# Optimization experiments

Measured on AMD Instinct MI355X. Metric: run time of the kernel, lower is better.

The kernel has to match this reference:

```python
import jax, jax.numpy as jnp
import numpy as np

B, P, D, H, L = 1024, 22, 3, 64, 4
HS = P + 1  # 22-dim one-hot atom type + 1 time channel
N = B * P


def _edges():
    # fully-connected directed edges (no self loops) per graph, batched with node offsets
    idx = np.arange(P)
    r, c = np.meshgrid(idx, idx, indexing='ij')
    m = r != c
    r0, c0 = r[m], c[m]
    off = (P * np.arange(B))[:, None]
    row = (r0[None, :] + off).reshape(-1)
    col = (c0[None, :] + off).reshape(-1)
    return row.astype(np.int32), col.astype(np.int32)


def setup_inputs() -> dict:
    key = jax.random.key(0)
    ks = jax.random.split(key, 12)
    s = 0.02
    row, col = _edges()
    return dict(
        input_array=jax.random.normal(ks[0], (B, P * D), jnp.float32),
        time_array=jax.random.uniform(ks[1], (B,), jnp.float32),
        emb_w=jax.random.normal(ks[2], (HS, H), jnp.float32) * s,
        emb_b=jnp.zeros((H,), jnp.float32),
        edge_w1=jax.random.normal(ks[3], (L, 2 * H + 2, H), jnp.float32) * s,
        edge_b1=jnp.zeros((L, H), jnp.float32),
        edge_w2=jax.random.normal(ks[4], (L, H, H), jnp.float32) * s,
        edge_b2=jnp.zeros((L, H), jnp.float32),
        node_w1=jax.random.normal(ks[5], (L, 2 * H, H), jnp.float32) * s,
        node_b1=jnp.zeros((L, H), jnp.float32),
        node_w2=jax.random.normal(ks[6], (L, H, H), jnp.float32) * s,
        node_b2=jnp.zeros((L, H), jnp.float32),
        cm_w1=jax.random.normal(ks[7], (L, H, H), jnp.float32) * s,
        cm_b1=jnp.zeros((L, H), jnp.float32),
        cm_w2=jax.random.normal(ks[8], (L, H, 1), jnp.float32) * 0.001,  # xavier gain=0.001 final layer
        cc_w1=jax.random.normal(ks[9], (L, H, H), jnp.float32) * s,
        cc_b1=jnp.zeros((L, H), jnp.float32),
        cc_w2=jax.random.normal(ks[10], (L, H, 1), jnp.float32) * 0.001,
        row=jnp.asarray(row),
        col=jnp.asarray(col),
    )


def reference(input_array, time_array, emb_w, emb_b, edge_w1, edge_b1, edge_w2, edge_b2,
              node_w1, node_b1, node_w2, node_b2, cm_w1, cm_b1, cm_w2,
              cc_w1, cc_b1, cc_w2, row, col):
    silu = jax.nn.silu
    x0 = input_array.reshape(N, D)
    # h_initial: one-hot atom types repeated over batch, plus time channel
    h = jnp.tile(jnp.eye(P, dtype=input_array.dtype), (B, 1))  # [N, 22]
    t = jnp.repeat(time_array[:, None], P, axis=1).reshape(N, 1)
    h = jnp.concatenate([h, t], axis=1)  # [N, 23]
    # edge_attr = squared distance at initial coords (fixed across layers)
    edge_attr = jnp.sum((x0[row] - x0[col]) ** 2, axis=1, keepdims=True)  # [E,1]
    h = h @ emb_w + emb_b  # embedding
    x = x0
    seg = lambda d: jax.ops.segment_sum(d, row, num_segments=N)
    for l in range(L):
        diff = x[row] - x[col]                                   # [E,3]
        radial = jnp.sum(diff ** 2, axis=1, keepdims=True)       # [E,1]
        coord_diff = diff / (jnp.sqrt(radial + 1e-8) + 1)
        e_in = jnp.concatenate([h[row], h[col], radial, edge_attr], axis=1)
        ef = silu(silu(e_in @ edge_w1[l] + edge_b1[l]) @ edge_w2[l] + edge_b2[l])  # [E,H]
        cross = jnp.cross(x[row], x[col])                        # [E,3]
        cross = cross / (jnp.sqrt(jnp.sum(cross ** 2, axis=1, keepdims=True) + 1e-8) + 1)
        cm = silu(ef @ cm_w1[l] + cm_b1[l]) @ cm_w2[l]           # [E,1]
        cc = silu(ef @ cc_w1[l] + cc_b1[l]) @ cc_w2[l]           # [E,1]
        trans = coord_diff * cm + cc * cross                     # [E,3]
        x = x + seg(trans)                                       # agg='sum'
        agg = jnp.concatenate([h, seg(ef)], axis=1)              # [N,2H]
        h = h + (silu(agg @ node_w1[l] + node_b1[l]) @ node_w2[l] + node_b2[l])  # recurrent
    vel = (x - x0).reshape(B, P, D)
    vel = vel - jnp.mean(vel, axis=1, keepdims=True)  # remove_mean
    return vel.reshape(B, P * D)
```

## Files before the change

### kernel.cpp

```cpp
#include <hip/hip_runtime.h>
#include <hip/hip_bf16.h>
#include <math.h>

#define PP 22
#define HH 64
#define NL 4
#define NE 462
#define NTILE 29
#define SST 68

typedef __attribute__((ext_vector_type(8))) short bf16x8;
typedef __attribute__((ext_vector_type(4))) float f32x4;

#define MFMA(A, B, C) __builtin_amdgcn_mfma_f32_16x16x32_bf16(A, B, C, 0, 0, 0)
#define PHI(mt, r) ((((mt) >> 1) << 5) + (((r) >> 2) << 3) + (((mt) & 1) << 2) + ((r) & 3))
#define WAVE_SYNC() asm volatile("s_waitcnt lgkmcnt(0)" ::: "memory")

__device__ __forceinline__ float silu_f(float v) { return v / (1.0f + __expf(-v)); }

__device__ __forceinline__ unsigned short f2bf(float x) {
    __hip_bfloat16 h = __float2bfloat16(x);
    unsigned short u;
    __builtin_memcpy(&u, &h, 2);
    return u;
}

#define LD8(dst, PTR) { \
    float4 _a = *(const float4*)(PTR); float4 _b = *(const float4*)((PTR) + 4); \
    dst[0]=_a.x; dst[1]=_a.y; dst[2]=_a.z; dst[3]=_a.w; \
    dst[4]=_b.x; dst[5]=_b.y; dst[6]=_b.z; dst[7]=_b.w; }

__global__ __launch_bounds__(64) void prep_w(
    const float* __restrict__ edge_w1, const float* __restrict__ edge_w2,
    const float* __restrict__ cm_w1, const float* __restrict__ cc_w1,
    const float* __restrict__ node_w1, const float* __restrict__ node_w2,
    unsigned short* __restrict__ ws)
{
    int blk = blockIdx.x;
    int l = blk >> 6, moff = blk & 63;
    int lane = threadIdx.x, n0 = lane & 15, kg = lane >> 4;
    const float* base; int col, kt;
    if (moff < 8)       { kt = moff >> 2;              int nt = moff & 3;        base = edge_w1 + l * 130 * HH;           col = nt * 16 + n0; }
    else if (moff < 16) { int m = moff - 8;  kt = m >> 2; int nt = m & 3;        base = edge_w1 + l * 130 * HH + 64 * HH; col = nt * 16 + n0; }
    else if (moff < 24) { int m = moff - 16; kt = m >> 2; int mt = m & 3;        base = edge_w2 + l * HH * HH;            col = PHI(mt, n0); }
    else if (moff < 32) { int m = moff - 24; kt = m >> 2; int nt = m & 3;        base = cm_w1 + l * HH * HH;              col = nt * 16 + n0; }
    else if (moff < 40) { int m = moff - 32; kt = m >> 2; int nt = m & 3;        base = cc_w1 + l * HH * HH;              col = nt * 16 + n0; }
    else if (moff < 56) { int m = moff - 40; kt = m >> 2; int mt = m & 3;        base = node_w1 + l * 128 * HH;           col = PHI(mt, n0); }
    else                { int m = moff - 56; kt = m >> 2; int nt = m & 3;        base = node_w2 + l * HH * HH;            col = nt * 16 + n0; }
    int k0 = kt * 32 + kg * 8;
    unsigned short* d = ws + blk * 512 + lane * 8;
#pragma unroll
    for (int j = 0; j < 8; ++j) d[j] = f2bf(base[(k0 + j) * HH + col]);
}

__global__ __launch_bounds__(512, 2) void egnn_kernel(
    const float* __restrict__ input, const float* __restrict__ timev,
    const float* __restrict__ emb_w, const float* __restrict__ emb_b,
    const float* __restrict__ edge_w1, const float* __restrict__ edge_b1,
    const float* __restrict__ edge_b2,
    const float* __restrict__ node_b1, const float* __restrict__ node_b2,
    const float* __restrict__ cm_b1, const float* __restrict__ cm_w2,
    const float* __restrict__ cc_b1, const float* __restrict__ cc_w2,
    const unsigned short* __restrict__ wfr,
    float* __restrict__ out)
{
    const int g0   = blockIdx.x * 2;
    const int tid  = threadIdx.x;
    const int w    = tid >> 6;
    const int lw   = w & 3;
    const int gi   = w >> 2;
    const int lane = tid & 63;
    const int n0   = lane & 15;
    const int kg   = lane >> 4;

    __shared__ __align__(16) unsigned short wlds[12288];
    __shared__ float sApre[2][PP][SST], sBpre[2][PP][SST];
    __shared__ float sh[2][PP][SST], sSeg[2][PP][SST];
    __shared__ __align__(16) float sx[2][PP][4];
    __shared__ __align__(16) float sx0[2][PP][4];
    __shared__ float sTr[2][PP][4];
    __shared__ float sW128[HH], sW129[HH];
    __shared__ float sBp[128];
    __shared__ float sHC[256];
    __shared__ float swPm[8][16], swPc[8][16];
    __shared__ float smean[2][3];

#define STAGE(SRC, N16) { const uint4* _s = (const uint4*)(SRC); uint4* _d = (uint4*)wlds; \
    for (int idx = tid; idx < (N16); idx += 512) _d[idx] = _s[idx]; }

    if (tid < 2 * PP * 3) {
        int gg = tid / (PP * 3), j = tid % (PP * 3);
        float v = input[(g0 + gg) * (PP * 3) + j];
        sx0[gg][j / 3][j % 3] = v;
        sx [gg][j / 3][j % 3] = v;
    }
    if (tid < 2 * PP) { int gg = tid / PP, p = tid % PP; sx0[gg][p][3] = 0.f; sx[gg][p][3] = 0.f; }
    {
        float tg = timev[g0 + gi];
        for (int i = lw; i < PP; i += 4)
            sh[gi][i][lane] = emb_w[i * HH + lane] + tg * emb_w[PP * HH + lane] + emb_b[lane];
    }
    for (int idx = tid; idx < 2 * PP * SST; idx += 512) (&sSeg[0][0][0])[idx] = 0.f;
    if (tid < 2 * PP * 4) (&sTr[0][0][0])[tid] = 0.f;
    __syncthreads();

    for (int l = 0; l < NL; ++l) {
        const unsigned short* wfl = wfr + (size_t)l * 32768;

        STAGE(wfl, 1024);
        if (tid < HH)               sW128[tid]        = edge_w1[(l * 130 + 128) * HH + tid];
        else if (tid < 2 * HH)      sW129[tid - HH]   = edge_w1[(l * 130 + 129) * HH + tid - HH];
        else if (tid < 2 * HH + 128) {
            int t2 = tid - 2 * HH;
            int i = t2 & 63, mt = i >> 4, r = i & 15;
            int phi = PHI(mt, r);
            sBp[t2] = (t2 < 64) ? edge_b2[l * HH + phi] : node_b1[l * HH + phi];
        } else if (tid < 2 * HH + 128 + 256) {
            int t3 = tid - (2 * HH + 128);
            int i = t3 & 63, arr = t3 >> 6;
            const float* src = (arr == 0) ? cm_b1 : (arr == 1) ? cc_b1 : (arr == 2) ? cm_w2 : cc_w2;
            sHC[t3] = src[l * HH + i];
        }
        __syncthreads();

        {
            int mtn = lw & 1, mat = lw >> 1;
            int node = mtn * 16 + n0;
            bool vn = node < PP;
            int crow = vn ? node : 0;
            bf16x8 hhi[2];
#pragma unroll
            for (int kt = 0; kt < 2; ++kt) {
                float vv[8];
                LD8(vv, &sh[gi][crow][kt * 32 + kg * 8]);
#pragma unroll
                for (int j = 0; j < 8; ++j)
                    hhi[kt][j] = (short)f2bf(vn ? vv[j] : 0.f);
            }
#pragma unroll
            for (int ntf = 0; ntf < 4; ++ntf) {
                f32x4 acc = (f32x4){0.f, 0.f, 0.f, 0.f};
#pragma unroll
                for (int kt = 0; kt < 2; ++kt) {
                    bf16x8 wv = *(const bf16x8*)&wlds[(mat * 8 + kt * 4 + ntf) * 512 + lane * 8];
                    acc = MFMA(hhi[kt], wv, acc);
                }
                int col = ntf * 16 + n0;
                float b1v = edge_b1[l * HH + col];
#pragma unroll
                for (int q = 0; q < 4; ++q) {
                    int m = mtn * 16 + kg * 4 + q;
                    if (m < PP) {
                        if (mat == 0) sApre[gi][m][col] = acc[q] + b1v;
                        else          sBpre[gi][m][col] = acc[q];
                    }
                }
            }
        }
        __syncthreads();

        STAGE(wfl + 16 * 512, 1536);
        __syncthreads();

        for (int jt = lw; jt < NTILE; jt += 4) {
            int e0 = jt * 16;
            int e = e0 + n0;
            bool vr = e < NE;
            int ec = vr ? e : (NE - 1);
            int a = ec % PP, r = ec / PP;
            int b = (r < a) ? r : r + 1;
            float4 xa = *(const float4*)&sx[gi][a][0];
            float4 xb = *(const float4*)&sx[gi][b][0];
            float4 oa = *(const float4*)&sx0[gi][a][0];
            float4 ob = *(const float4*)&sx0[gi][b][0];
            float dx = xa.x - xb.x, dy = xa.y - xb.y, dz = xa.z - xb.z;
            float rad = dx * dx + dy * dy + dz * dz;
            float ex = oa.x - ob.x, ey = oa.y - ob.y, ez = oa.z - ob.z;
            float ea = ex * ex + ey * ey + ez * ez;
            float inv = 1.0f / (sqrtf(rad + 1e-8f) + 1.0f);
            float cdx = dx * inv, cdy = dy * inv, cdz = dz * inv;
            float cx = xa.y * xb.z - xa.z * xb.y;
            float cy = xa.z * xb.x - xa.x * xb.z;
            float cz = xa.x * xb.y - xa.y * xb.x;
            float cn = 1.0f / (sqrtf(cx * cx + cy * cy + cz * cz + 1e-8f) + 1.0f);
            float crx = cx * cn, cry = cy * cn, crz = cz * cn;

            f32x4 acc[4];
#pragma unroll
            for (int mt = 0; mt < 4; ++mt) acc[mt] = (f32x4){0.f, 0.f, 0.f, 0.f};
#pragma unroll
            for (int kt = 0; kt < 2; ++kt) {
                int base = kt * 32 + kg * 8;
                float av[8], bv[8], w8[8], w9[8];
                LD8(av, &sApre[gi][a][base]);
                LD8(bv, &sBpre[gi][b][base]);
                LD8(w8, &sW128[base]);
                LD8(w9, &sW129[base]);
                bf16x8 zhi;
#pragma unroll
                for (int j8 = 0; j8 < 8; ++j8) {
                    float z = av[j8] + bv[j8] + rad * w8[j8] + ea * w9[j8];
                    zhi[j8] = (short)f2bf(silu_f(z));
                }
#pragma unroll
                for (int mt = 0; mt < 4; ++mt) {
                    bf16x8 wv = *(const bf16x8*)&wlds[(kt * 4 + mt) * 512 + lane * 8];
                    acc[mt] = MFMA(wv, zhi, acc[mt]);
                }
            }
            unsigned short pkE[4][4];
#pragma unroll
            for (int mt = 0; mt < 4; ++mt) {
                int phib = ((mt >> 1) << 5) + (kg << 3) + ((mt & 1) << 2);
#pragma unroll
                for (int q = 0; q < 4; ++q) {
                    float v = silu_f(acc[mt][q] + sBp[mt * 16 + kg * 4 + q]);
                    v = vr ? v : 0.f;
                    pkE[mt][q] = f2bf(v);
                    if (vr) atomicAdd(&sSeg[gi][a][phib + q], v);
                }
            }
            bf16x8 ehi[2];
#pragma unroll
            for (int kt = 0; kt < 2; ++kt)
#pragma unroll
                for (int j8 = 0; j8 < 8; ++j8)
                    ehi[kt][j8] = (short)pkE[kt * 2 + (j8 >> 2)][j8 & 3];

            float pm[4] = {0.f, 0.f, 0.f, 0.f}, pc[4] = {0.f, 0.f, 0.f, 0.f};
#pragma unroll
            for (int nt = 0; nt < 4; ++nt) {
                f32x4 am = (f32x4){0.f, 0.f, 0.f, 0.f};
                f32x4 ac = (f32x4){0.f, 0.f, 0.f, 0.f};
#pragma unroll
                for (int kt = 0; kt < 2; ++kt) {
                    bf16x8 cmw = *(const bf16x8*)&wlds[(8 + kt * 4 + nt) * 512 + lane * 8];
                    bf16x8 ccw = *(const bf16x8*)&wlds[(16 + kt * 4 + nt) * 512 + lane * 8];
                    am = MFMA(ehi[kt], cmw, am);
                    ac = MFMA(ehi[kt], ccw, ac);
                }
                float cmb = sHC[nt * 16 + n0];
                float ccb = sHC[64 + nt * 16 + n0];
                float cm2 = sHC[128 + nt * 16 + n0];
                float cc2 = sHC[192 + nt * 16 + n0];
#pragma unroll
                for (int q = 0; q < 4; ++q) {
                    pm[q] += silu_f(am[q] + cmb) * cm2;
                    pc[q] += silu_f(ac[q] + ccb) * cc2;
                }
            }
#pragma unroll
            for (int q = 0; q < 4; ++q) {
#pragma unroll
                for (int off = 1; off <= 8; off <<= 1) {
                    pm[q] += __shfl_xor(pm[q], off);
                    pc[q] += __shfl_xor(pc[q], off);
                }
            }
            if (n0 == 0) {
#pragma unroll
                for (int q = 0; q < 4; ++q) {
                    swPm[w][kg * 4 + q] = pm[q];
                    swPc[w][kg * 4 + q] = pc[q];
                }
            }
            WAVE_SYNC();
            float pmv = swPm[w][n0];
            float pcv = swPc[w][n0];
            if (kg == 0 && vr) {
                atomicAdd(&sTr[gi][a][0], cdx * pmv + pcv * crx);
                atomicAdd(&sTr[gi][a][1], cdy * pmv + pcv * cry);
                atomicAdd(&sTr[gi][a][2], cdz * pmv + pcv * crz);
            }
            WAVE_SYNC();
        }
        __syncthreads();

        STAGE(wfl + 40 * 512, 1536);
        __syncthreads();

        unsigned short pkN[4][4];
        {
            int mtn = lw >> 1;
            int node = mtn * 16 + n0;
            bool vn = node < PP;
            int crow = vn ? node : 0;
            f32x4 acc[4];
#pragma unroll
            for (int mt = 0; mt < 4; ++mt) acc[mt] = (f32x4){0.f, 0.f, 0.f, 0.f};
#pragma unroll
            for (int kt = 0; kt < 4; ++kt) {
                const float* srcp = (kt < 2) ? &sh[gi][crow][kt * 32 + kg * 8]
                                             : &sSeg[gi][crow][(kt - 2) * 32 + kg * 8];
                float vv[8];
                LD8(vv, srcp);
                bf16x8 bhi;
#pragma unroll
                for (int j8 = 0; j8 < 8; ++j8)
                    bhi[j8] = (short)f2bf(vn ? vv[j8] : 0.f);
#pragma unroll
                for (int mt = 0; mt < 4; ++mt) {
                    bf16x8 wv = *(const bf16x8*)&wlds[(kt * 4 + mt) * 512 + lane * 8];
                    acc[mt] = MFMA(wv, bhi, acc[mt]);
                }
            }
#pragma unroll
            for (int mt = 0; mt < 4; ++mt)
#pragma unroll
                for (int q = 0; q < 4; ++q)
                    pkN[mt][q] = f2bf(silu_f(acc[mt][q] + sBp[64 + mt * 16 + kg * 4 + q]));
        }
        __syncthreads();

        {
            bf16x8 mh[2];
#pragma unroll
            for (int kt = 0; kt < 2; ++kt)
#pragma unroll
                for (int j8 = 0; j8 < 8; ++j8)
                    mh[kt][j8] = (short)pkN[kt * 2 + (j8 >> 2)][j8 & 3];
            int mtn = lw >> 1;
#pragma unroll
            for (int t = 0; t < 2; ++t) {
                int ntf = (lw & 1) * 2 + t;
                f32x4 acc = (f32x4){0.f, 0.f, 0.f, 0.f};
#pragma unroll
                for (int kt = 0; kt < 2; ++kt) {
                    bf16x8 wv = *(const bf16x8*)&wlds[(16 + kt * 4 + ntf) * 512 + lane * 8];
                    acc = MFMA(mh[kt], wv, acc);
                }
                int col = ntf * 16 + n0;
                float nb2 = node_b2[l * HH + col];
#pragma unroll
                for (int q = 0; q < 4; ++q) {
                    int m = mtn * 16 + kg * 4 + q;
                    if (m < PP) sh[gi][m][col] += acc[q] + nb2;
                }
            }
        }
        if (tid < 2 * PP * 4) {
            int gg = tid / (PP * 4), j = tid % (PP * 4);
            int p = j >> 2, d = j & 3;
            float v = sTr[gg][p][d];
            if (d < 3) sx[gg][p][d] += v;
            sTr[gg][p][d] = 0.f;
        }
        for (int idx = tid; idx < 2 * PP * SST; idx += 512) (&sSeg[0][0][0])[idx] = 0.f;
        __syncthreads();
    }

    if (tid < 6) {
        int gg = tid / 3, d = tid % 3;
        float s = 0.0f;
        for (int p = 0; p < PP; ++p) s += sx[gg][p][d] - sx0[gg][p][d];
        smean[gg][d] = s / (float)PP;
    }
    __syncthreads();
    if (tid < 2 * PP * 3) {
        int gg = tid / (PP * 3), j = tid % (PP * 3);
        int p = j / 3, d = j % 3;
        out[(g0 + gg) * (PP * 3) + j] = (sx[gg][p][d] - sx0[gg][p][d]) - smean[gg][d];
    }
#undef STAGE
}

extern "C" void kernel_launch(void* const* d_in, const int* in_sizes, int n_in,
                              void* d_out, int out_size, void* d_ws, size_t ws_size,
                              hipStream_t stream) {
    const float* input   = (const float*)d_in[0];
    const float* timev   = (const float*)d_in[1];
    const float* emb_w   = (const float*)d_in[2];
    const float* emb_b   = (const float*)d_in[3];
    const float* edge_w1 = (const float*)d_in[4];
    const float* edge_b1 = (const float*)d_in[5];
    const float* edge_w2 = (const float*)d_in[6];
    const float* edge_b2 = (const float*)d_in[7];
    const float* node_w1 = (const float*)d_in[8];
    const float* node_b1 = (const float*)d_in[9];
    const float* node_w2 = (const float*)d_in[10];
    const float* node_b2 = (const float*)d_in[11];
    const float* cm_w1   = (const float*)d_in[12];
    const float* cm_b1   = (const float*)d_in[13];
    const float* cm_w2   = (const float*)d_in[14];
    const float* cc_w1   = (const float*)d_in[15];
    const float* cc_b1   = (const float*)d_in[16];
    const float* cc_w2   = (const float*)d_in[17];

    unsigned short* wsu = (unsigned short*)d_ws;
    prep_w<<<dim3(NL * 64), dim3(64), 0, stream>>>(edge_w1, edge_w2, cm_w1, cc_w1,
                                                   node_w1, node_w2, wsu);

    float* out = (float*)d_out;
    egnn_kernel<<<dim3(512), dim3(512), 0, stream>>>(
        input, timev, emb_w, emb_b, edge_w1, edge_b1, edge_b2,
        node_b1, node_b2, cm_b1, cm_w2, cc_b1, cc_w2, wsu, out);
}
```

Before: 877.4 us.

## Process four graphs per block with 1024 threads to share staged weights

Each block now handles four molecular graphs instead of two, runs 1024 threads, and launches half as many blocks. Per-graph shared arrays and the loop bounds are resized to match. The aim is to spread each layer's weight staging into LDS, and the block-wide barriers, over more graphs. In exchange, launch bounds drop to one block per CU and the per-block LDS footprint roughly doubles, which lowers occupancy and lengthens each barrier. The elided middle section also has to be correct for the new wave-to-graph mapping.

```diff
diff --git a/kernel.cpp b/kernel.cpp
--- a/kernel.cpp
+++ b/kernel.cpp
@@ -8,6 +8,7 @@
 #define NE 462
 #define NTILE 29
 #define SST 68
+#define NG 4
 
 typedef __attribute__((ext_vector_type(8))) short bf16x8;
 typedef __attribute__((ext_vector_type(4))) float f32x4;
@@ -53,7 +54,7 @@
     for (int j = 0; j < 8; ++j) d[j] = f2bf(base[(k0 + j) * HH + col]);
 }
 
-__global__ __launch_bounds__(512, 2) void egnn_kernel(
+__global__ __launch_bounds__(1024, 1) void egnn_kernel(
     const float* __restrict__ input, const float* __restrict__ timev,
     const float* __restrict__ emb_w, const float* __restrict__ emb_b,
     const float* __restrict__ edge_w1, const float* __restrict__ edge_b1,
@@ -64,7 +65,7 @@
     const unsigned short* __restrict__ wfr,
     float* __restrict__ out)
 {
-    const int g0   = blockIdx.x * 2;
+    const int g0   = blockIdx.x * NG;
     const int tid  = threadIdx.x;
     const int w    = tid >> 6;
     const int lw   = w & 3;
@@ -74,34 +75,34 @@
     const int kg   = lane >> 4;
 
     __shared__ __align__(16) unsigned short wlds[12288];
-    __shared__ float sApre[2][PP][SST], sBpre[2][PP][SST];
-    __shared__ float sh[2][PP][SST], sSeg[2][PP][SST];
-    __shared__ __align__(16) float sx[2][PP][4];
-    __shared__ __align__(16) float sx0[2][PP][4];
-    __shared__ float sTr[2][PP][4];
+    __shared__ float sApre[NG][PP][SST], sBpre[NG][PP][SST];
+    __shared__ float sh[NG][PP][SST], sSeg[NG][PP][SST];
+    __shared__ __align__(16) float sx[NG][PP][4];
+    __shared__ __align__(16) float sx0[NG][PP][4];
+    __shared__ float sTr[NG][PP][4];
     __shared__ float sW128[HH], sW129[HH];
     __shared__ float sBp[128];
     __shared__ float sHC[256];
-    __shared__ float swPm[8][16], swPc[8][16];
-    __shared__ float smean[2][3];
+    __shared__ float swPm[16][16], swPc[16][16];
+    __shared__ float smean[NG][3];
 
 #define STAGE(SRC, N16) { const uint4* _s = (const uint4*)(SRC); uint4* _d = (uint4*)wlds; \
-    for (int idx = tid; idx < (N16); idx += 512) _d[idx] = _s[idx]; }
-
-    if (tid < 2 * PP * 3) {
+    for (int idx = tid; idx < (N16); idx += 1024) _d[idx] = _s[idx]; }
+
+    if (tid < NG * PP * 3) {
         int gg = tid / (PP * 3), j = tid % (PP * 3);
         float v = input[(g0 + gg) * (PP * 3) + j];
         sx0[gg][j / 3][j % 3] = v;
         sx [gg][j / 3][j % 3] = v;
     }
-    if (tid < 2 * PP) { int gg = tid / PP, p = tid % PP; sx0[gg][p][3] = 0.f; sx[gg][p][3] = 0.f; }
+    if (tid < NG * PP) { int gg = tid / PP, p = tid % PP; sx0[gg][p][3] = 0.f; sx[gg][p][3] = 0.f; }
     {
         float tg = timev[g0 + gi];
         for (int i = lw; i < PP; i += 4)
             sh[gi][i][lane] = emb_w[i * HH + lane] + tg * emb_w[PP * HH + lane] + emb_b[lane];
     }
-    for (int idx = tid; idx < 2 * PP * SST; idx += 512) (&sSeg[0][0][0])[idx] = 0.f;
-    if (tid < 2 * PP * 4) (&sTr[0][0][0])[tid] = 0.f;
+    for (int idx = tid; idx < NG * PP * SST; idx += 1024) (&sSeg[0][0][0])[idx] = 0.f;
+    if (tid < NG * PP * 4) (&sTr[0][0][0])[tid] = 0.f;
     __syncthreads();
 
     for (int l = 0; l < NL; ++l) {
@@ -338,25 +339,25 @@
                 }
             }
         }
-        if (tid < 2 * PP * 4) {
+        if (tid < NG * PP * 4) {
             int gg = tid / (PP * 4), j = tid % (PP * 4);
             int p = j >> 2, d = j & 3;
             float v = sTr[gg][p][d];
             if (d < 3) sx[gg][p][d] += v;
             sTr[gg][p][d] = 0.f;
         }
-        for (int idx = tid; idx < 2 * PP * SST; idx += 512) (&sSeg[0][0][0])[idx] = 0.f;
-        __syncthreads();
-    }
-
-    if (tid < 6) {
+        for (int idx = tid; idx < NG * PP * SST; idx += 1024) (&sSeg[0][0][0])[idx] = 0.f;
+        __syncthreads();
+    }
+
+    if (tid < NG * 3) {
         int gg = tid / 3, d = tid % 3;
         float s = 0.0f;
         for (int p = 0; p < PP; ++p) s += sx[gg][p][d] - sx0[gg][p][d];
         smean[gg][d] = s / (float)PP;
     }
     __syncthreads();
-    if (tid < 2 * PP * 3) {
+    if (tid < NG * PP * 3) {
         int gg = tid / (PP * 3), j = tid % (PP * 3);
         int p = j / 3, d = j % 3;
         out[(g0 + gg) * (PP * 3) + j] = (sx[gg][p][d] - sx0[gg][p][d]) - smean[gg][d];
@@ -391,7 +392,7 @@
                                                    node_w1, node_w2, wsu);
 
     float* out = (float*)d_out;
-    egnn_kernel<<<dim3(512), dim3(512), 0, stream>>>(
+    egnn_kernel<<<dim3(1024 / NG), dim3(1024), 0, stream>>>(
         input, timev, emb_w, emb_b, edge_w1, edge_b1, edge_b2,
         node_b1, node_b2, cm_b1, cm_w2, cc_b1, cc_w2, wsu, out);
 }
```

After: 817.9 us. 6.8% less time.
